# Kernel tuning notes

Measured on AMD Instinct MI355X. Metric: run time of the kernel, lower is better.

## Reference

```python
import jax, jax.numpy as jnp
import numpy as np

N_NODES = 100000
N_EDGES = 1600000
D_IN = 128
D_HID = 128
D_PROJ = 128
D_DEC = 512
BN_EPS = 1e-5
ENC_SLOPE = 0.5
DEC_SLOPE = 0.01


def _leaky(x, slope):
    return jnp.where(x >= 0, x, slope * x)


def setup_inputs() -> dict:
    key = jax.random.key(0)
    ks = jax.random.split(key, 12)
    glorot = lambda k, shp: jax.random.normal(k, shp, jnp.float32) * (1.0 / np.sqrt(shp[-1]))
    return {
        "x": jax.random.normal(ks[0], (N_NODES, D_IN), jnp.float32),
        "edge_index": jax.random.randint(ks[1], (2, N_EDGES), 0, N_NODES, jnp.int64),
        # SAGEConv: lin_l (neighbor aggr, with bias), lin_r (root, no bias)
        "Wl": glorot(ks[2], (D_HID, D_IN)),
        "bl": jnp.zeros((D_HID,), jnp.float32),
        "Wr": glorot(ks[3], (D_HID, D_IN)),
        # projection head: Linear + PReLU
        "Wp": glorot(ks[4], (D_PROJ, D_HID)),
        "bp": jnp.zeros((D_PROJ,), jnp.float32),
        "a_prelu": jnp.asarray(0.25, jnp.float32),
        # decoder: Linear -> BN -> LeakyReLU -> Linear
        "Wd1": glorot(ks[5], (D_DEC, D_HID)),
        "bd1": jnp.zeros((D_DEC,), jnp.float32),
        "gamma": jnp.ones((D_DEC,), jnp.float32),
        "beta": jnp.zeros((D_DEC,), jnp.float32),
        "Wd2": glorot(ks[6], (D_IN, D_DEC)),
        "bd2": jnp.zeros((D_IN,), jnp.float32),
    }


def reference(x, edge_index, Wl, bl, Wr, Wp, bp, a_prelu, Wd1, bd1, gamma, beta, Wd2, bd2):
    n = x.shape[0]
    src, dst = edge_index[0], edge_index[1]
    # SAGEConv mean aggregation: gather source features, segment-mean at dst
    msg_sum = jax.ops.segment_sum(x[src], dst, num_segments=n)   # [N, D_IN]
    cnt = jax.ops.segment_sum(jnp.ones((src.shape[0],), x.dtype), dst, num_segments=n)
    aggr = msg_sum / jnp.maximum(cnt, 1.0)[:, None]              # isolated nodes -> 0
    h = aggr @ Wl.T + bl + x @ Wr.T                              # lin_l(aggr) + lin_r(x)
    h = _leaky(h, ENC_SLOPE)                                     # encoder LeakyReLU(0.5)
    # projection head: Linear + PReLU
    zp = h @ Wp.T + bp
    z = jnp.where(zp >= 0, zp, a_prelu * zp)
    # decoder: Linear -> BatchNorm1d (training batch stats, biased var) -> LeakyReLU -> Linear
    d = h @ Wd1.T + bd1
    mu = jnp.mean(d, axis=0)
    var = jnp.mean(jnp.square(d - mu), axis=0)
    d = (d - mu) * jax.lax.rsqrt(var + BN_EPS) * gamma + beta
    d = _leaky(d, DEC_SLOPE)
    rec = d @ Wd2.T + bd2
    target = x
    return (h, z, rec, target)
```

## Files before the change

kernel.cpp:

```cpp
#include <hip/hip_runtime.h>
#include <cstdint>
#include <cstddef>

#define D 128
#define DDEC 512

typedef __attribute__((ext_vector_type(8))) short short8;
typedef __attribute__((ext_vector_type(4))) float f32x4;

__device__ __forceinline__ ushort f2bf(float f) {
  uint32_t u = __float_as_uint(f);
  u = u + 0x7FFF + ((u >> 16) & 1);
  return (ushort)(u >> 16);
}
__device__ __forceinline__ float bf2f(ushort u) {
  return __uint_as_float(((uint32_t)u) << 16);
}

__global__ void detect_i64(const int* __restrict__ ei, int* __restrict__ flag) {
  if (threadIdx.x == 0 && blockIdx.x == 0) {
    int allz = 1;
    for (int k = 0; k < 64; ++k)
      if (ei[2 * k + 1] != 0) { allz = 0; break; }
    *flag = allz ? 2 : 1;
  }
}

__global__ __launch_bounds__(256) void prep_count_kernel(
    const float* __restrict__ x, const float* __restrict__ Wl,
    const float* __restrict__ Wr, const float* __restrict__ Wp,
    const float* __restrict__ Wd1, const float* __restrict__ Wd2,
    const int* __restrict__ ei,
    ushort* __restrict__ xb, ushort* __restrict__ wb,
    float* __restrict__ tgt,
    int* __restrict__ deg, const int* __restrict__ flag,
    int n8, int xblocks, int E)
{
  int b = blockIdx.x;
  if (b < xblocks) {
    int i = b * 256 + threadIdx.x;
    if (i >= n8) return;
    const float* s = x + (size_t)i * 8;
    float4 f0 = *(const float4*)s;
    float4 f1 = *(const float4*)(s + 4);
    short8 v;
    v[0] = (short)f2bf(f0.x); v[1] = (short)f2bf(f0.y);
    v[2] = (short)f2bf(f0.z); v[3] = (short)f2bf(f0.w);
    v[4] = (short)f2bf(f1.x); v[5] = (short)f2bf(f1.y);
    v[6] = (short)f2bf(f1.z); v[7] = (short)f2bf(f1.w);
    *(short8*)&xb[(size_t)i * 8] = v;
    if (tgt) {
      *(float4*)&tgt[(size_t)i * 8] = f0;
      *(float4*)&tgt[(size_t)i * 8 + 4] = f1;
    }
  } else if (b < xblocks + 704) {
    int i = (b - xblocks) * 256 + threadIdx.x;
    if (i >= 180224) return;
    float v;
    if (i < 16384) v = Wl[i];
    else if (i < 32768) v = Wr[i - 16384];
    else if (i < 49152) v = Wp[i - 32768];
    else if (i < 114688) v = Wd1[i - 49152];
    else v = Wd2[i - 114688];
    wb[i] = f2bf(v);
  } else {
    int e = (b - xblocks - 704) * 256 + threadIdx.x;
    if (e >= E) return;
    int s = *flag;
    int dst = ei[((long long)E + e) * s];
    atomicAdd(&deg[dst], 1);
  }
}

__global__ __launch_bounds__(256) void scan_reduce(
    const int* __restrict__ deg, int* __restrict__ bsum, int N)
{
  __shared__ int red[256];
  int base = blockIdx.x * 1024 + threadIdx.x * 4;
  int s = 0;
#pragma unroll
  for (int k = 0; k < 4; ++k) { int i = base + k; if (i < N) s += deg[i]; }
  red[threadIdx.x] = s;
  __syncthreads();
  for (int off = 128; off > 0; off >>= 1) {
    if (threadIdx.x < off) red[threadIdx.x] += red[threadIdx.x + off];
    __syncthreads();
  }
  if (threadIdx.x == 0) bsum[blockIdx.x] = red[0];
}

__global__ void scan_bsum(int* __restrict__ bsum, int* __restrict__ rowptr,
                          int NB, int N, int E)
{
  __shared__ int tmp[256];
  int t = threadIdx.x;
  int v = (t < NB) ? bsum[t] : 0;
  tmp[t] = v;
  __syncthreads();
  for (int off = 1; off < 256; off <<= 1) {
    int add = (t >= off) ? tmp[t - off] : 0;
    __syncthreads();
    tmp[t] += add;
    __syncthreads();
  }
  if (t < NB) bsum[t] = tmp[t] - v;
  if (t == 0) rowptr[N] = E;
}

__global__ __launch_bounds__(256) void scan_final(
    const int* __restrict__ deg, const int* __restrict__ bsum,
    int* __restrict__ rowptr, int N)
{
  __shared__ int tsum[256];
  int base = blockIdx.x * 1024 + threadIdx.x * 4;
  int loc[4]; int s = 0;
#pragma unroll
  for (int k = 0; k < 4; ++k) { int i = base + k; loc[k] = (i < N) ? deg[i] : 0; s += loc[k]; }
  tsum[threadIdx.x] = s;
  __syncthreads();
  for (int off = 1; off < 256; off <<= 1) {
    int add = (threadIdx.x >= off) ? tsum[threadIdx.x - off] : 0;
    __syncthreads();
    tsum[threadIdx.x] += add;
    __syncthreads();
  }
  int excl = tsum[threadIdx.x] - s + bsum[blockIdx.x];
#pragma unroll
  for (int k = 0; k < 4; ++k) {
    int i = base + k;
    if (i < N) { rowptr[i] = excl; excl += loc[k]; }
  }
}

__global__ __launch_bounds__(256) void fill_csr(
    const int* __restrict__ ei, const int* __restrict__ rowptr,
    int* __restrict__ fillc, int* __restrict__ colidx,
    const int* __restrict__ flag, int E)
{
  int e = blockIdx.x * 256 + threadIdx.x;
  if (e >= E) return;
  int s = *flag;
  int src = ei[(long long)e * s];
  int dst = ei[((long long)E + e) * s];
  int pos = rowptr[dst] + atomicAdd(&fillc[dst], 1);
  colidx[pos] = src;
}

__global__ __launch_bounds__(256) void aggregate_kernel(
    const int* __restrict__ rowptr, const int* __restrict__ colidx,
    const ushort* __restrict__ xb, ushort* __restrict__ aggrb, int N)
{
  int wave = (blockIdx.x * 256 + threadIdx.x) >> 6;
  int lane = threadIdx.x & 63;
  if (wave >= N) return;
  int s = rowptr[wave], epos = rowptr[wave + 1];
  float ax = 0.f, ay = 0.f;
  int e = s;
  for (; e + 3 < epos; e += 4) {
    int s0 = colidx[e], s1 = colidx[e + 1], s2 = colidx[e + 2], s3 = colidx[e + 3];
    uint u0 = *(const uint*)&xb[(size_t)s0 * D + lane * 2];
    uint u1 = *(const uint*)&xb[(size_t)s1 * D + lane * 2];
    uint u2 = *(const uint*)&xb[(size_t)s2 * D + lane * 2];
    uint u3 = *(const uint*)&xb[(size_t)s3 * D + lane * 2];
    ax += __uint_as_float(u0 << 16) + __uint_as_float(u1 << 16)
        + __uint_as_float(u2 << 16) + __uint_as_float(u3 << 16);
    ay += __uint_as_float(u0 & 0xFFFF0000u) + __uint_as_float(u1 & 0xFFFF0000u)
        + __uint_as_float(u2 & 0xFFFF0000u) + __uint_as_float(u3 & 0xFFFF0000u);
  }
  for (; e < epos; ++e) {
    uint u0 = *(const uint*)&xb[(size_t)colidx[e] * D + lane * 2];
    ax += __uint_as_float(u0 << 16);
    ay += __uint_as_float(u0 & 0xFFFF0000u);
  }
  int degn = epos - s;
  float inv = 1.0f / (float)(degn > 0 ? degn : 1);
  uint out = ((uint)f2bf(ax * inv)) | (((uint)f2bf(ay * inv)) << 16);
  *(uint*)&aggrb[(size_t)wave * D + lane * 2] = out;
}

__device__ __forceinline__ void mma_tile_g(const ushort* __restrict__ A, size_t ald,
                                           const ushort* __restrict__ B, size_t bld,
                                           f32x4 acc[4][4], int lane)
{
  const int r = lane & 15, g = lane >> 4;
#pragma unroll
  for (int ks = 0; ks < 4; ++ks) {
    short8 a[4], b[4];
#pragma unroll
    for (int m = 0; m < 4; ++m)
      a[m] = *(const short8*)&A[(size_t)(m * 16 + r) * ald + ks * 32 + g * 8];
#pragma unroll
    for (int n = 0; n < 4; ++n)
      b[n] = *(const short8*)&B[(size_t)(n * 16 + r) * bld + ks * 32 + g * 8];
#pragma unroll
    for (int m = 0; m < 4; ++m)
#pragma unroll
      for (int n = 0; n < 4; ++n)
        acc[m][n] = __builtin_amdgcn_mfma_f32_16x16x32_bf16(a[m], b[n], acc[m][n], 0, 0, 0);
  }
}

__device__ __forceinline__ void mma_tile_l(const ushort* aLds,
                                           const ushort* __restrict__ bGlb, size_t bld,
                                           f32x4 acc[4][4], int lane)
{
  const int r = lane & 15, g = lane >> 4;
#pragma unroll
  for (int ks = 0; ks < 4; ++ks) {
    short8 a[4], b[4];
#pragma unroll
    for (int m = 0; m < 4; ++m)
      a[m] = *(const short8*)&aLds[(m * 16 + r) * 136 + ks * 32 + g * 8];
#pragma unroll
    for (int n = 0; n < 4; ++n)
      b[n] = *(const short8*)&bGlb[(size_t)(n * 16 + r) * bld + ks * 32 + g * 8];
#pragma unroll
    for (int m = 0; m < 4; ++m)
#pragma unroll
      for (int n = 0; n < 4; ++n)
        acc[m][n] = __builtin_amdgcn_mfma_f32_16x16x32_bf16(a[m], b[n], acc[m][n], 0, 0, 0);
  }
}

__device__ __forceinline__ void mma_tile_l_T(const ushort* aLds,
                                             const ushort* __restrict__ bGlb, size_t bld,
                                             f32x4 acc[4][4], int lane)
{
  const int r = lane & 15, g = lane >> 4;
#pragma unroll
  for (int ks = 0; ks < 4; ++ks) {
    short8 a[4], b[4];
#pragma unroll
    for (int m = 0; m < 4; ++m)
      a[m] = *(const short8*)&aLds[(m * 16 + r) * 136 + ks * 32 + g * 8];
#pragma unroll
    for (int n = 0; n < 4; ++n)
      b[n] = *(const short8*)&bGlb[(size_t)(n * 16 + r) * bld + ks * 32 + g * 8];
#pragma unroll
    for (int m = 0; m < 4; ++m)
#pragma unroll
      for (int n = 0; n < 4; ++n)
        acc[m][n] = __builtin_amdgcn_mfma_f32_16x16x32_bf16(b[n], a[m], acc[m][n], 0, 0, 0);
  }
}

__device__ __forceinline__ void stage128(const float* __restrict__ src, int N,
                                         int row0, ushort* lds, int t)
{
#pragma unroll
  for (int p = 0; p < 8; ++p) {
    int r = (t >> 4) + p * 16;
    int c = (t & 15) * 8;
    short8 v = {};
    int row = row0 + r;
    if (row < N) {
      const float* s = src + (size_t)row * D + c;
      float4 f0 = *(const float4*)s;
      float4 f1 = *(const float4*)(s + 4);
      v[0] = (short)f2bf(f0.x); v[1] = (short)f2bf(f0.y);
      v[2] = (short)f2bf(f0.z); v[3] = (short)f2bf(f0.w);
      v[4] = (short)f2bf(f1.x); v[5] = (short)f2bf(f1.y);
      v[6] = (short)f2bf(f1.z); v[7] = (short)f2bf(f1.w);
    }
    *(short8*)&lds[r * 136 + c] = v;
  }
}

__global__ __launch_bounds__(256, 3) void gemm_hz_dstat(
    const ushort* __restrict__ aggrb, const ushort* __restrict__ xb,
    const ushort* __restrict__ Wlb, const ushort* __restrict__ Wrb,
    const ushort* __restrict__ Wpb, const ushort* __restrict__ Wd1b,
    const float* __restrict__ bl, const float* __restrict__ bp,
    const float* __restrict__ ap,
    float* __restrict__ h, ushort* __restrict__ hb, float* __restrict__ z,
    float* __restrict__ sums, float* __restrict__ sumsq, int N)
{
  __shared__ ushort Hs[128 * 136];
  __shared__ float part1[2][8][132];
  __shared__ float part2[2][8][132];
  const int t = threadIdx.x;
  const int row0 = blockIdx.x * 128;
  const int lane = t & 63, w = t >> 6;
  const int wm = w >> 1, wn = w & 1;
  const int g = lane >> 4, cr = lane & 15;
  {
    f32x4 acc[4][4] = {};
    mma_tile_g(aggrb + (size_t)(row0 + wm * 64) * D, D, Wlb + (size_t)(wn * 64) * D, D, acc, lane);
    mma_tile_g(xb + (size_t)(row0 + wm * 64) * D, D, Wrb + (size_t)(wn * 64) * D, D, acc, lane);
#pragma unroll
    for (int n = 0; n < 4; ++n) {
      int col = wn * 64 + n * 16 + cr;
      float b = bl[col];
#pragma unroll
      for (int m = 0; m < 4; ++m)
#pragma unroll
        for (int rr = 0; rr < 4; ++rr) {
          int lrow = wm * 64 + m * 16 + g * 4 + rr;
          float v = acc[m][n][rr] + b;
          v = (v >= 0.f) ? v : 0.5f * v;
          Hs[lrow * 136 + col] = f2bf(v);
        }
    }
  }
  __syncthreads();
#pragma unroll
  for (int p = 0; p < 8; ++p) {
    int idx = t + p * 256;
    int r = idx >> 4, c = (idx & 15) * 8;
    int row = row0 + r;
    if (row < N) {
      short8 v = *(short8*)&Hs[r * 136 + c];
      *(short8*)&hb[(size_t)row * D + c] = v;
      float4 f0, f1;
      f0.x = bf2f((ushort)v[0]); f0.y = bf2f((ushort)v[1]);
      f0.z = bf2f((ushort)v[2]); f0.w = bf2f((ushort)v[3]);
      f1.x = bf2f((ushort)v[4]); f1.y = bf2f((ushort)v[5]);
      f1.z = bf2f((ushort)v[6]); f1.w = bf2f((ushort)v[7]);
      *(float4*)&h[(size_t)row * D + c] = f0;
      *(float4*)&h[(size_t)row * D + c + 4] = f1;
    }
  }
  {
    f32x4 zacc[4][4] = {};
    mma_tile_l_T(Hs + wm * 64 * 136, Wpb + (size_t)(wn * 64) * D, D, zacc, lane);
    const float alpha = ap[0];
#pragma unroll
    for (int m = 0; m < 4; ++m) {
      int row = row0 + wm * 64 + m * 16 + cr;
      if (row < N) {
#pragma unroll
        for (int n = 0; n < 4; ++n) {
          int col = wn * 64 + n * 16 + g * 4;
          float4 bv = *(const float4*)&bp[col];
          float4 o;
          float v0 = zacc[m][n][0] + bv.x; o.x = (v0 >= 0.f) ? v0 : alpha * v0;
          float v1 = zacc[m][n][1] + bv.y; o.y = (v1 >= 0.f) ? v1 : alpha * v1;
          float v2 = zacc[m][n][2] + bv.z; o.z = (v2 >= 0.f) ? v2 : alpha * v2;
          float v3 = zacc[m][n][3] + bv.w; o.w = (v3 >= 0.f) ? v3 : alpha * v3;
          *(float4*)&z[(size_t)row * D + col] = o;
        }
      }
    }
  }
  for (int cc = 0; cc < 4; ++cc) {
    int c0 = cc * 128;
    int pb = cc & 1;
    f32x4 dacc[4][4] = {};
    mma_tile_l(Hs + wm * 64 * 136, Wd1b + (size_t)(c0 + wn * 64) * D, D, dacc, lane);
#pragma unroll
    for (int n = 0; n < 4; ++n) {
      float s1 = 0.f, s2 = 0.f;
#pragma unroll
      for (int m = 0; m < 4; ++m)
#pragma unroll
        for (int rr = 0; rr < 4; ++rr) {
          int row = row0 + wm * 64 + m * 16 + g * 4 + rr;
          if (row < N) {
            float v = dacc[m][n][rr];
            s1 += v; s2 += v * v;
          }
        }
      part1[pb][wm * 4 + g][wn * 64 + n * 16 + cr] = s1;
      part2[pb][wm * 4 + g][wn * 64 + n * 16 + cr] = s2;
    }
    __syncthreads();
    if (t < 128) {
      float s = 0;
#pragma unroll
      for (int k = 0; k < 8; ++k) s += part1[pb][k][t];
      atomicAdd(&sums[c0 + t], s);
    } else {
      int c = t - 128;
      float s = 0;
#pragma unroll
      for (int k = 0; k < 8; ++k) s += part2[pb][k][c];
      atomicAdd(&sumsq[c0 + c], s);
    }
  }
}

__global__ void finalize_kernel(
    const float* __restrict__ sums, const float* __restrict__ sumsq,
    const float* __restrict__ gamma, const float* __restrict__ beta,
    float* __restrict__ scale, float* __restrict__ shift, int N)
{
  int c = blockIdx.x * blockDim.x + threadIdx.x;
  if (c < DDEC) {
    float inv_n = 1.0f / (float)N;
    float mu = sums[c] * inv_n;
    float var = sumsq[c] * inv_n - mu * mu;
    float sc = gamma[c] * rsqrtf(var + 1e-5f);
    scale[c] = sc;
    shift[c] = beta[c] - mu * sc;
  }
}

__global__ __launch_bounds__(256, 2) void rec_mfma(
    const ushort* __restrict__ hb, const ushort* __restrict__ Wd1b,
    const ushort* __restrict__ Wd2b,
    const float* __restrict__ scale, const float* __restrict__ shift,
    const float* __restrict__ bd2, float* __restrict__ rec, int N)
{
  __shared__ ushort Hs[128 * 136];
  __shared__ ushort Dn[128 * 136];
  const int t = threadIdx.x;
  const int row0 = blockIdx.x * 128;
#pragma unroll
  for (int p = 0; p < 8; ++p) {
    int idx = t + p * 256;
    int r = idx >> 4, c = (idx & 15) * 8;
    short8 v = *(const short8*)&hb[(size_t)(row0 + r) * D + c];
    *(short8*)&Hs[r * 136 + c] = v;
  }
  const int lane = t & 63, w = t >> 6;
  const int wm = w >> 1, wn = w & 1;
  const int g = lane >> 4, cr = lane & 15;
  f32x4 acc[4][4] = {};
  __syncthreads();
  for (int c0 = 0; c0 < DDEC; c0 += 128) {
    f32x4 dacc[4][4] = {};
    mma_tile_l(Hs + wm * 64 * 136, Wd1b + (size_t)(c0 + wn * 64) * D, D, dacc, lane);
    __syncthreads();
#pragma unroll
    for (int n = 0; n < 4; ++n) {
      int lc = wn * 64 + n * 16 + cr;
      int c = c0 + lc;
      float sc = scale[c], sh = shift[c];
#pragma unroll
      for (int m = 0; m < 4; ++m)
#pragma unroll
        for (int rr = 0; rr < 4; ++rr) {
          float v = dacc[m][n][rr] * sc + sh;
          v = (v >= 0.f) ? v : 0.01f * v;
          Dn[(wm * 64 + m * 16 + g * 4 + rr) * 136 + lc] = f2bf(v);
        }
    }
    __syncthreads();
    mma_tile_l_T(Dn + wm * 64 * 136, Wd2b + (size_t)(wn * 64) * DDEC + c0, DDEC, acc, lane);
  }
#pragma unroll
  for (int m = 0; m < 4; ++m) {
    int row = row0 + wm * 64 + m * 16 + cr;
    if (row < N) {
#pragma unroll
      for (int n = 0; n < 4; ++n) {
        int col = wn * 64 + n * 16 + g * 4;
        float4 bv = *(const float4*)&bd2[col];
        float4 o;
        o.x = acc[m][n][0] + bv.x;
        o.y = acc[m][n][1] + bv.y;
        o.z = acc[m][n][2] + bv.z;
        o.w = acc[m][n][3] + bv.w;
        *(float4*)&rec[(size_t)row * D + col] = o;
      }
    }
  }
}

__global__ __launch_bounds__(256, 3) void gemm_h_mfma(
    const ushort* __restrict__ aggrb, const ushort* __restrict__ xb,
    const ushort* __restrict__ Wlb, const ushort* __restrict__ Wrb,
    const float* __restrict__ bl, float* __restrict__ h,
    ushort* __restrict__ hb, int N)
{
  const int t = threadIdx.x;
  const int row0 = blockIdx.x * 128;
  const int lane = t & 63, w = t >> 6;
  const int wm = w >> 1, wn = w & 1;
  f32x4 acc[4][4] = {};
  mma_tile_g(aggrb + (size_t)(row0 + wm * 64) * D, D, Wlb + (size_t)(wn * 64) * D, D, acc, lane);
  mma_tile_g(xb + (size_t)(row0 + wm * 64) * D, D, Wrb + (size_t)(wn * 64) * D, D, acc, lane);
  const int g = lane >> 4, cr = lane & 15;
#pragma unroll
  for (int n = 0; n < 4; ++n) {
    int col = wn * 64 + n * 16 + cr;
    float b = bl[col];
#pragma unroll
    for (int m = 0; m < 4; ++m)
#pragma unroll
      for (int rr = 0; rr < 4; ++rr) {
        int row = row0 + wm * 64 + m * 16 + g * 4 + rr;
        if (row < N) {
          float v = acc[m][n][rr] + b;
          v = (v >= 0.f) ? v : 0.5f * v;
          h[(size_t)row * D + col] = v;
          hb[(size_t)row * D + col] = f2bf(v);
        }
      }
  }
}

__global__ __launch_bounds__(256, 4) void dstat_mfma(
    const ushort* __restrict__ hb, const ushort* __restrict__ Wd1b,
    float* __restrict__ sums, float* __restrict__ sumsq, int N)
{
  __shared__ float part1[8][132];
  __shared__ float part2[8][132];
  const int t = threadIdx.x;
  const int row0 = blockIdx.x * 128;
  const int lane = t & 63, w = t >> 6;
  const int wm = w >> 1, wn = w & 1;
  const int g = lane >> 4, cr = lane & 15;
  for (int c0 = 0; c0 < DDEC; c0 += 128) {
    f32x4 dacc[4][4] = {};
    mma_tile_g(hb + (size_t)(row0 + wm * 64) * D, D,
               Wd1b + (size_t)(c0 + wn * 64) * D, D, dacc, lane);
#pragma unroll
    for (int n = 0; n < 4; ++n) {
      float s1 = 0.f, s2 = 0.f;
#pragma unroll
      for (int m = 0; m < 4; ++m)
#pragma unroll
        for (int rr = 0; rr < 4; ++rr) {
          int row = row0 + wm * 64 + m * 16 + g * 4 + rr;
          if (row < N) {
            float v = dacc[m][n][rr];
            s1 += v; s2 += v * v;
          }
        }
      part1[wm * 4 + g][wn * 64 + n * 16 + cr] = s1;
      part2[wm * 4 + g][wn * 64 + n * 16 + cr] = s2;
    }
    __syncthreads();
    if (t < 128) {
      float s = 0;
#pragma unroll
      for (int k = 0; k < 8; ++k) s += part1[k][t];
      atomicAdd(&sums[c0 + t], s);
    } else {
      int c = t - 128;
      float s = 0;
#pragma unroll
      for (int k = 0; k < 8; ++k) s += part2[k][c];
      atomicAdd(&sumsq[c0 + c], s);
    }
    __syncthreads();
  }
}

__global__ __launch_bounds__(256, 2) void rec_mfma_fb(
    const ushort* __restrict__ hb, const ushort* __restrict__ Wd1b,
    const ushort* __restrict__ Wd2b,
    const float* __restrict__ scale, const float* __restrict__ shift,
    const float* __restrict__ bd2, float* __restrict__ rec, int N)
{
  __shared__ ushort Hs[128 * 136];
  __shared__ ushort Dn[128 * 136];
  const int t = threadIdx.x;
  const int row0 = blockIdx.x * 128;
#pragma unroll
  for (int p = 0; p < 8; ++p) {
    int idx = t + p * 256;
    int r = idx >> 4, c = (idx & 15) * 8;
    short8 v = *(const short8*)&hb[(size_t)(row0 + r) * D + c];
    *(short8*)&Hs[r * 136 + c] = v;
  }
  const int lane = t & 63, w = t >> 6;
  const int wm = w >> 1, wn = w & 1;
  const int g = lane >> 4, cr = lane & 15;
  f32x4 acc[4][4] = {};
  __syncthreads();
  for (int c0 = 0; c0 < DDEC; c0 += 128) {
    f32x4 dacc[4][4] = {};
    mma_tile_l(Hs + wm * 64 * 136, Wd1b + (size_t)(c0 + wn * 64) * D, D, dacc, lane);
    __syncthreads();
#pragma unroll
    for (int n = 0; n < 4; ++n) {
      int lc = wn * 64 + n * 16 + cr;
      int c = c0 + lc;
      float sc = scale[c], sh = shift[c];
#pragma unroll
      for (int m = 0; m < 4; ++m)
#pragma unroll
        for (int rr = 0; rr < 4; ++rr) {
          float v = dacc[m][n][rr] * sc + sh;
          v = (v >= 0.f) ? v : 0.01f * v;
          Dn[(wm * 64 + m * 16 + g * 4 + rr) * 136 + lc] = f2bf(v);
        }
    }
    __syncthreads();
    mma_tile_l(Dn + wm * 64 * 136, Wd2b + (size_t)(wn * 64) * DDEC + c0, DDEC, acc, lane);
  }
#pragma unroll
  for (int n = 0; n < 4; ++n) {
    int col = wn * 64 + n * 16 + cr;
    float b = bd2[col];
#pragma unroll
    for (int m = 0; m < 4; ++m)
#pragma unroll
      for (int rr = 0; rr < 4; ++rr) {
        int row = row0 + wm * 64 + m * 16 + g * 4 + rr;
        if (row < N) rec[(size_t)row * D + col] = acc[m][n][rr] + b;
      }
  }
}

__global__ __launch_bounds__(256, 2) void gemm_z_staged(
    const float* __restrict__ h, const ushort* __restrict__ Wpb,
    const float* __restrict__ bp, const float* __restrict__ ap,
    float* __restrict__ z, int N)
{
  __shared__ ushort As[128 * 136];
  const int t = threadIdx.x;
  const int row0 = blockIdx.x * 128;
  stage128(h, N, row0, As, t);
  __syncthreads();
  const int lane = t & 63, w = t >> 6;
  const int wm = w >> 1, wn = w & 1;
  f32x4 acc[4][4] = {};
  mma_tile_l(As + wm * 64 * 136, Wpb + (size_t)(wn * 64) * D, D, acc, lane);
  const float alpha = ap[0];
  const int g = lane >> 4, cr = lane & 15;
#pragma unroll
  for (int n = 0; n < 4; ++n) {
    int col = wn * 64 + n * 16 + cr;
    float b = bp[col];
#pragma unroll
    for (int m = 0; m < 4; ++m)
#pragma unroll
      for (int rr = 0; rr < 4; ++rr) {
        int row = row0 + wm * 64 + m * 16 + g * 4 + rr;
        if (row < N) {
          float v = acc[m][n][rr] + b;
          z[(size_t)row * D + col] = (v >= 0.f) ? v : alpha * v;
        }
      }
  }
}

extern "C" void kernel_launch(void* const* d_in, const int* in_sizes, int n_in,
                              void* d_out, int out_size, void* d_ws, size_t ws_size,
                              hipStream_t stream)
{
  const float* x   = (const float*)d_in[0];
  const int*   ei  = (const int*)d_in[1];
  const float* Wl  = (const float*)d_in[2];
  const float* bl  = (const float*)d_in[3];
  const float* Wr  = (const float*)d_in[4];
  const float* Wp  = (const float*)d_in[5];
  const float* bp  = (const float*)d_in[6];
  const float* ap  = (const float*)d_in[7];
  const float* Wd1 = (const float*)d_in[8];
  const float* bd1 = (const float*)d_in[9];
  const float* gm  = (const float*)d_in[10];
  const float* bt  = (const float*)d_in[11];
  const float* Wd2 = (const float*)d_in[12];
  const float* bd2 = (const float*)d_in[13];
  (void)bd1;

  const int N = in_sizes[0] / D;
  const int E = in_sizes[1] / 2;

  float* h_out   = (float*)d_out;
  float* z_out   = h_out + (size_t)N * D;
  float* rec_out = z_out + (size_t)N * D;
  float* tgt_out = rec_out + (size_t)N * D;

  const size_t ws_need = ((size_t)3 * N + E + 4096) * 4
                       + (size_t)3 * N * D * 2 + 360448
                       + ((size_t)N + 128) * DDEC * 2 + 2048;
  const bool usews = ws_size >= ws_need;

  int *deg, *fillc, *bsum, *flag, *rowptr, *colidx;
  float *sums, *sumsq, *scale, *shift;
  ushort *xb, *hb, *aggrb, *wb;

  if (usews) {
    deg    = (int*)d_ws;
    fillc  = deg + N;
    sums   = (float*)(fillc + N);
    sumsq  = sums + 512;
    scale  = sumsq + 512;
    shift  = scale + 512;
    bsum   = (int*)(shift + 512);
    flag   = bsum + 256;
    rowptr = flag + 16;
    colidx = rowptr + (N + 16);
    xb     = (ushort*)(((uintptr_t)(colidx + E) + 255) & ~(uintptr_t)255);
    hb     = xb + (size_t)N * D;
    aggrb  = hb + (size_t)N * D;
    wb     = aggrb + (size_t)N * D;
  } else {
    sums   = (float*)d_ws;
    sumsq  = sums + DDEC;
    scale  = sumsq + DDEC;
    shift  = scale + DDEC;
    flag   = (int*)(shift + DDEC);
    bsum   = flag + 1;
    colidx = (int*)tgt_out;
    deg    = colidx + E;
    fillc  = deg + N;
    rowptr = fillc + N;
    xb     = (ushort*)(tgt_out + 2000000);
    wb     = (ushort*)(tgt_out + 8500000);
    aggrb  = (ushort*)z_out;
    hb     = aggrb + (size_t)N * D;
  }
  ushort* Wlb  = wb;
  ushort* Wrb  = wb + 16384;
  ushort* Wpb  = wb + 32768;
  ushort* Wd1b = wb + 49152;
  ushort* Wd2b = wb + 114688;

  if (usews) {
    hipMemsetAsync(deg, 0, (size_t)(2 * N + 1024) * sizeof(int), stream);
  } else {
    hipMemsetAsync(deg, 0, (size_t)2 * N * sizeof(int), stream);
    hipMemsetAsync(sums, 0, (size_t)2 * DDEC * sizeof(float), stream);
  }

  detect_i64<<<1, 64, 0, stream>>>(ei, flag);

  int n8 = N * (D / 8);
  int xblocks = (n8 + 255) / 256;
  int eb = (E + 255) / 256;
  prep_count_kernel<<<xblocks + 704 + eb, 256, 0, stream>>>(
      x, Wl, Wr, Wp, Wd1, Wd2, ei, xb, wb,
      usews ? tgt_out : nullptr, deg, flag, n8, xblocks, E);

  int NB = (N + 1023) / 1024;
  scan_reduce<<<NB, 256, 0, stream>>>(deg, bsum, N);
  scan_bsum<<<1, 256, 0, stream>>>(bsum, rowptr, NB, N, E);
  scan_final<<<NB, 256, 0, stream>>>(deg, bsum, rowptr, N);

  fill_csr<<<eb, 256, 0, stream>>>(ei, rowptr, fillc, colidx, flag, E);

  long long ag_threads = (long long)N * 64;
  aggregate_kernel<<<(int)((ag_threads + 255) / 256), 256, 0, stream>>>(
      rowptr, colidx, xb, aggrb, N);

  int rb = (N + 127) / 128;
  if (usews) {
    gemm_hz_dstat<<<rb, 256, 0, stream>>>(aggrb, xb, Wlb, Wrb, Wpb, Wd1b,
                                          bl, bp, ap, h_out, hb, z_out,
                                          sums, sumsq, N);
    finalize_kernel<<<2, 256, 0, stream>>>(sums, sumsq, gm, bt, scale, shift, N);
    rec_mfma<<<rb, 256, 0, stream>>>(hb, Wd1b, Wd2b, scale, shift, bd2, rec_out, N);
  } else {
    gemm_h_mfma<<<rb, 256, 0, stream>>>(aggrb, xb, Wlb, Wrb, bl, h_out, hb, N);
    dstat_mfma<<<rb, 256, 0, stream>>>(hb, Wd1b, sums, sumsq, N);
    finalize_kernel<<<2, 256, 0, stream>>>(sums, sumsq, gm, bt, scale, shift, N);
    rec_mfma_fb<<<rb, 256, 0, stream>>>(hb, Wd1b, Wd2b, scale, shift, bd2, rec_out, N);
    gemm_z_staged<<<rb, 256, 0, stream>>>(h_out, Wpb, bp, ap, z_out, N);
    hipMemcpyAsync(tgt_out, x, (size_t)N * D * sizeof(float), hipMemcpyDeviceToDevice, stream);
  }
}
```

Baseline: 435.0 us.

## Unroll gather by 8, shuffle-reduce BN stats, per-wave rec kernel

The aggregate loop now issues eight neighbor gathers per iteration instead of four, exposing more memory-level parallelism. gemm_hz_dstat replaces its LDS partial-sum buffers and block barrier with wave shuffles and per-lane atomics, and its occupancy hint rises from 3 to 4. The reconstruction kernel is rewritten so that each wave owns 32 rows, with a private LDS scratch and no block-wide barriers inside the loop, and it targets occupancy 3. The trade-off is more global atomics and repeated per-wave reloads of Wd1/Wd2 from global memory, with possible register pressure at the higher occupancy targets.

```diff
diff --git a/kernel.cpp b/kernel.cpp
--- a/kernel.cpp
+++ b/kernel.cpp
@@ -156,16 +156,18 @@
   int s = rowptr[wave], epos = rowptr[wave + 1];
   float ax = 0.f, ay = 0.f;
   int e = s;
-  for (; e + 3 < epos; e += 4) {
-    int s0 = colidx[e], s1 = colidx[e + 1], s2 = colidx[e + 2], s3 = colidx[e + 3];
-    uint u0 = *(const uint*)&xb[(size_t)s0 * D + lane * 2];
-    uint u1 = *(const uint*)&xb[(size_t)s1 * D + lane * 2];
-    uint u2 = *(const uint*)&xb[(size_t)s2 * D + lane * 2];
-    uint u3 = *(const uint*)&xb[(size_t)s3 * D + lane * 2];
-    ax += __uint_as_float(u0 << 16) + __uint_as_float(u1 << 16)
-        + __uint_as_float(u2 << 16) + __uint_as_float(u3 << 16);
-    ay += __uint_as_float(u0 & 0xFFFF0000u) + __uint_as_float(u1 & 0xFFFF0000u)
-        + __uint_as_float(u2 & 0xFFFF0000u) + __uint_as_float(u3 & 0xFFFF0000u);
+  for (; e + 7 < epos; e += 8) {
+    int sx[8];
+#pragma unroll
+    for (int k = 0; k < 8; ++k) sx[k] = colidx[e + k];
+    uint u[8];
+#pragma unroll
+    for (int k = 0; k < 8; ++k) u[k] = *(const uint*)&xb[(size_t)sx[k] * D + lane * 2];
+#pragma unroll
+    for (int k = 0; k < 8; ++k) {
+      ax += __uint_as_float(u[k] << 16);
+      ay += __uint_as_float(u[k] & 0xFFFF0000u);
+    }
   }
   for (; e < epos; ++e) {
     uint u0 = *(const uint*)&xb[(size_t)colidx[e] * D + lane * 2];
@@ -266,7 +268,7 @@
   }
 }
 
-__global__ __launch_bounds__(256, 3) void gemm_hz_dstat(
+__global__ __launch_bounds__(256, 4) void gemm_hz_dstat(
     const ushort* __restrict__ aggrb, const ushort* __restrict__ xb,
     const ushort* __restrict__ Wlb, const ushort* __restrict__ Wrb,
     const ushort* __restrict__ Wpb, const ushort* __restrict__ Wd1b,
@@ -276,8 +278,6 @@
     float* __restrict__ sums, float* __restrict__ sumsq, int N)
 {
   __shared__ ushort Hs[128 * 136];
-  __shared__ float part1[2][8][132];
-  __shared__ float part2[2][8][132];
   const int t = threadIdx.x;
   const int row0 = blockIdx.x * 128;
   const int lane = t & 63, w = t >> 6;
@@ -344,7 +344,6 @@
   }
   for (int cc = 0; cc < 4; ++cc) {
     int c0 = cc * 128;
-    int pb = cc & 1;
     f32x4 dacc[4][4] = {};
     mma_tile_l(Hs + wm * 64 * 136, Wd1b + (size_t)(c0 + wn * 64) * D, D, dacc, lane);
 #pragma unroll
@@ -360,21 +359,13 @@
             s1 += v; s2 += v * v;
           }
         }
-      part1[pb][wm * 4 + g][wn * 64 + n * 16 + cr] = s1;
-      part2[pb][wm * 4 + g][wn * 64 + n * 16 + cr] = s2;
-    }
-    __syncthreads();
-    if (t < 128) {
-      float s = 0;
-#pragma unroll
-      for (int k = 0; k < 8; ++k) s += part1[pb][k][t];
-      atomicAdd(&sums[c0 + t], s);
-    } else {
-      int c = t - 128;
-      float s = 0;
-#pragma unroll
-      for (int k = 0; k < 8; ++k) s += part2[pb][k][c];
-      atomicAdd(&sumsq[c0 + c], s);
+      s1 += __shfl_xor(s1, 16); s1 += __shfl_xor(s1, 32);
+      s2 += __shfl_xor(s2, 16); s2 += __shfl_xor(s2, 32);
+      if (lane < 16) {
+        int col = c0 + wn * 64 + n * 16 + lane;
+        atomicAdd(&sums[col], s1);
+        atomicAdd(&sumsq[col], s2);
+      }
     }
   }
 }
@@ -395,56 +386,82 @@
   }
 }
 
-__global__ __launch_bounds__(256, 2) void rec_mfma(
+__global__ __launch_bounds__(256, 3) void rec_v3(
     const ushort* __restrict__ hb, const ushort* __restrict__ Wd1b,
     const ushort* __restrict__ Wd2b,
     const float* __restrict__ scale, const float* __restrict__ shift,
     const float* __restrict__ bd2, float* __restrict__ rec, int N)
 {
   __shared__ ushort Hs[128 * 136];
-  __shared__ ushort Dn[128 * 136];
+  __shared__ ushort DnAll[4][32 * 72];
   const int t = threadIdx.x;
   const int row0 = blockIdx.x * 128;
 #pragma unroll
   for (int p = 0; p < 8; ++p) {
     int idx = t + p * 256;
-    int r = idx >> 4, c = (idx & 15) * 8;
-    short8 v = *(const short8*)&hb[(size_t)(row0 + r) * D + c];
-    *(short8*)&Hs[r * 136 + c] = v;
-  }
+    int r0 = idx >> 4, c = (idx & 15) * 8;
+    short8 v = *(const short8*)&hb[(size_t)(row0 + r0) * D + c];
+    *(short8*)&Hs[r0 * 136 + c] = v;
+  }
+  __syncthreads();
   const int lane = t & 63, w = t >> 6;
-  const int wm = w >> 1, wn = w & 1;
-  const int g = lane >> 4, cr = lane & 15;
-  f32x4 acc[4][4] = {};
-  __syncthreads();
-  for (int c0 = 0; c0 < DDEC; c0 += 128) {
-    f32x4 dacc[4][4] = {};
-    mma_tile_l(Hs + wm * 64 * 136, Wd1b + (size_t)(c0 + wn * 64) * D, D, dacc, lane);
-    __syncthreads();
+  const int r = lane & 15, g = lane >> 4;
+  const int wrow0 = w * 32;
+  ushort* dn = DnAll[w];
+  f32x4 acc[2][8] = {};
+  for (int cc = 0; cc < 8; ++cc) {
+    const int c0 = cc * 64;
+    f32x4 dacc[2][4] = {};
+#pragma unroll
+    for (int ks = 0; ks < 4; ++ks) {
+      short8 a[2], b[4];
+#pragma unroll
+      for (int m = 0; m < 2; ++m)
+        a[m] = *(const short8*)&Hs[(wrow0 + m * 16 + r) * 136 + ks * 32 + g * 8];
+#pragma unroll
+      for (int n = 0; n < 4; ++n)
+        b[n] = *(const short8*)&Wd1b[(size_t)(c0 + n * 16 + r) * D + ks * 32 + g * 8];
+#pragma unroll
+      for (int m = 0; m < 2; ++m)
+#pragma unroll
+        for (int n = 0; n < 4; ++n)
+          dacc[m][n] = __builtin_amdgcn_mfma_f32_16x16x32_bf16(a[m], b[n], dacc[m][n], 0, 0, 0);
+    }
 #pragma unroll
     for (int n = 0; n < 4; ++n) {
-      int lc = wn * 64 + n * 16 + cr;
-      int c = c0 + lc;
-      float sc = scale[c], sh = shift[c];
-#pragma unroll
-      for (int m = 0; m < 4; ++m)
+      int cg = c0 + n * 16 + r;
+      float sc = scale[cg], sh = shift[cg];
+#pragma unroll
+      for (int m = 0; m < 2; ++m)
 #pragma unroll
         for (int rr = 0; rr < 4; ++rr) {
           float v = dacc[m][n][rr] * sc + sh;
           v = (v >= 0.f) ? v : 0.01f * v;
-          Dn[(wm * 64 + m * 16 + g * 4 + rr) * 136 + lc] = f2bf(v);
+          dn[(m * 16 + g * 4 + rr) * 72 + n * 16 + r] = f2bf(v);
         }
     }
-    __syncthreads();
-    mma_tile_l_T(Dn + wm * 64 * 136, Wd2b + (size_t)(wn * 64) * DDEC + c0, DDEC, acc, lane);
-  }
-#pragma unroll
-  for (int m = 0; m < 4; ++m) {
-    int row = row0 + wm * 64 + m * 16 + cr;
+#pragma unroll
+    for (int ks2 = 0; ks2 < 2; ++ks2) {
+      short8 a2[2];
+#pragma unroll
+      for (int m = 0; m < 2; ++m)
+        a2[m] = *(const short8*)&dn[(m * 16 + r) * 72 + ks2 * 32 + g * 8];
+#pragma unroll
+      for (int n = 0; n < 8; ++n) {
+        short8 b2 = *(const short8*)&Wd2b[(size_t)(n * 16 + r) * DDEC + c0 + ks2 * 32 + g * 8];
+#pragma unroll
+        for (int m = 0; m < 2; ++m)
+          acc[m][n] = __builtin_amdgcn_mfma_f32_16x16x32_bf16(b2, a2[m], acc[m][n], 0, 0, 0);
+      }
+    }
+  }
+#pragma unroll
+  for (int m = 0; m < 2; ++m) {
+    int row = row0 + wrow0 + m * 16 + r;
     if (row < N) {
 #pragma unroll
-      for (int n = 0; n < 4; ++n) {
-        int col = wn * 64 + n * 16 + g * 4;
+      for (int n = 0; n < 8; ++n) {
+        int col = n * 16 + g * 4;
         float4 bv = *(const float4*)&bd2[col];
         float4 o;
         o.x = acc[m][n][0] + bv.x;
@@ -735,7 +752,7 @@
                                           bl, bp, ap, h_out, hb, z_out,
                                           sums, sumsq, N);
     finalize_kernel<<<2, 256, 0, stream>>>(sums, sumsq, gm, bt, scale, shift, N);
-    rec_mfma<<<rb, 256, 0, stream>>>(hb, Wd1b, Wd2b, scale, shift, bd2, rec_out, N);
+    rec_v3<<<rb, 256, 0, stream>>>(hb, Wd1b, Wd2b, scale, shift, bd2, rec_out, N);
   } else {
     gemm_h_mfma<<<rb, 256, 0, stream>>>(aggrb, xb, Wlb, Wrb, bl, h_out, hb, N);
     dstat_mfma<<<rb, 256, 0, stream>>>(hb, Wd1b, sums, sumsq, N);
```

Result: slower. 580.2 us (+33.4%).
